# Performance work log

Measured on AMD Instinct MI355X. Metric: run time of the kernel, lower is better.

Reference implementation:

```python
import jax, jax.numpy as jnp
import numpy as np

N_NODES = 100000
N_EDGES = 3200000
D_IN = 256
D_HID = 256
D_OUT = 256


def _sage_conv(x, src, tgt, W_l, b_l, W_r):
    # PyG SAGEConv (aggr='mean', root_weight=True):
    #   out = lin_l(mean_{j in N(i)} x_j) + lin_r(x_i)
    n = x.shape[0]
    msgs = x[src]                                              # [E, d] gather
    agg = jax.ops.segment_sum(msgs, tgt, num_segments=n)       # [N, d] scatter-add
    deg = jax.ops.segment_sum(jnp.ones((src.shape[0],), x.dtype), tgt,
                              num_segments=n)                  # [N]
    agg = agg / jnp.maximum(deg, 1.0)[:, None]                 # mean aggregation
    return agg @ W_l + b_l + x @ W_r


def setup_inputs() -> dict:
    key = jax.random.key(0)
    ks = jax.random.split(key, 8)
    x = jax.random.normal(ks[0], (N_NODES, D_IN), dtype=jnp.float32)
    edge_index = jax.random.randint(ks[1], (2, N_EDGES), 0, N_NODES, dtype=jnp.int64)
    s1 = 1.0 / np.sqrt(D_IN)
    s2 = 1.0 / np.sqrt(D_HID)
    return {
        "x": x,
        "edge_index": edge_index,
        "W_l1": jax.random.uniform(ks[2], (D_IN, D_HID), jnp.float32, -s1, s1),
        "b1": jnp.zeros((D_HID,), jnp.float32),
        "W_r1": jax.random.uniform(ks[3], (D_IN, D_HID), jnp.float32, -s1, s1),
        "W_l2": jax.random.uniform(ks[4], (D_HID, D_OUT), jnp.float32, -s2, s2),
        "b2": jnp.zeros((D_OUT,), jnp.float32),
        "W_r2": jax.random.uniform(ks[5], (D_HID, D_OUT), jnp.float32, -s2, s2),
    }


def reference(x, edge_index, W_l1, b1, W_r1, W_l2, b2, W_r2):
    src, tgt = edge_index[0], edge_index[1]
    h = jax.nn.relu(_sage_conv(x, src, tgt, W_l1, b1, W_r1))   # layer 1 + relu
    # dropout p=0.0 -> identity
    logits = _sage_conv(h, src, tgt, W_l2, b2, W_r2)           # final layer
    return logits
```

## Files before the change

### kernel.cpp

```cpp
#include <hip/hip_runtime.h>
#include <hip/hip_bf16.h>
#include <cstdint>
#include <cstddef>

#define N_NODES 100000
#define N_EDGES 3200000
#define D 256
#define CAP 64
#define OVF_MAX (1 << 20)

typedef __attribute__((ext_vector_type(8))) short short8;
typedef __attribute__((ext_vector_type(4))) float f32x4;

__device__ inline unsigned short f2bf(float f) {
    unsigned int u = __float_as_uint(f);
    u += 0x7FFFu + ((u >> 16) & 1u);
    return (unsigned short)(u >> 16);
}
__device__ inline float bf2f(unsigned short h) {
    return __uint_as_float(((unsigned int)h) << 16);
}

__global__ void fill_bucket(const int* __restrict__ src,
                            const int* __restrict__ tgt,
                            int* __restrict__ cnt,
                            int* __restrict__ bucket,
                            int2* __restrict__ ovf,
                            int* __restrict__ ovf_cnt) {
    int e = blockIdx.x * blockDim.x + threadIdx.x;
    if (e >= N_EDGES) return;
    int t = tgt[e];
    int s = src[e];
    if (t >= 0 && t < N_NODES && s >= 0 && s < N_NODES) {
        int p = atomicAdd(&cnt[t], 1);
        if (p < CAP) {
            bucket[(size_t)t * CAP + p] = s;
        } else {
            int q = atomicAdd(ovf_cnt, 1);
            if (q < OVF_MAX) ovf[q] = make_int2(t, s);
        }
    }
}

__global__ __launch_bounds__(256) void convert_kernel(const float* __restrict__ in,
                                                      unsigned short* __restrict__ out,
                                                      int n8) {
    int i = blockIdx.x * 256 + threadIdx.x;
    if (i >= n8) return;
    const float4 a = ((const float4*)in)[i * 2 + 0];
    const float4 b = ((const float4*)in)[i * 2 + 1];
    short8 v;
    v[0] = (short)f2bf(a.x); v[1] = (short)f2bf(a.y);
    v[2] = (short)f2bf(a.z); v[3] = (short)f2bf(a.w);
    v[4] = (short)f2bf(b.x); v[5] = (short)f2bf(b.y);
    v[6] = (short)f2bf(b.z); v[7] = (short)f2bf(b.w);
    ((short8*)out)[i] = v;
}

__global__ __launch_bounds__(256) void pack_b_kernel(const float* __restrict__ Wl,
                                                     const float* __restrict__ Wr,
                                                     unsigned short* __restrict__ Bp) {
    int t = blockIdx.x * 256 + threadIdx.x;
    if (t >= 16384) return;
    int lane = t & 63, kb = (t >> 6) & 15, ntile = t >> 10;
    int n = ntile * 16 + (lane & 15);
    int kbase = kb * 32 + (lane >> 4) * 8;
    short8 v;
#pragma unroll
    for (int j = 0; j < 8; ++j) {
        int k = kbase + j;
        const float* W = (k < 256) ? Wl : Wr;
        v[j] = (short)f2bf(W[(size_t)(k & 255) * D + n]);
    }
    ((short8*)Bp)[t] = v;
}

__device__ inline void acc8(float& a0, float& a1, float& a2, float& a3,
                            float& a4, float& a5, float& a6, float& a7,
                            const short8& r) {
    a0 += bf2f((unsigned short)r[0]); a1 += bf2f((unsigned short)r[1]);
    a2 += bf2f((unsigned short)r[2]); a3 += bf2f((unsigned short)r[3]);
    a4 += bf2f((unsigned short)r[4]); a5 += bf2f((unsigned short)r[5]);
    a6 += bf2f((unsigned short)r[6]); a7 += bf2f((unsigned short)r[7]);
}

__global__ __launch_bounds__(256) void aggregate_bf16(
    const unsigned short* __restrict__ in, unsigned short* __restrict__ out,
    const int* __restrict__ cnt, const int* __restrict__ bucket,
    const int2* __restrict__ ovf, const int* __restrict__ ovf_cnt) {
    int node = blockIdx.x * 4 + (threadIdx.x >> 6);
    if (node >= N_NODES) return;
    const int lane = threadIdx.x & 63;
    const int half = lane >> 5;
    const int l32  = lane & 31;
    const int deg = cnt[node];
    const int inb = (deg < CAP) ? deg : CAP;
    const int* __restrict__ bk = bucket + (size_t)node * CAP;
    const unsigned short* __restrict__ rowp = in + (size_t)l32 * 8;

    float a0 = 0.f, a1 = 0.f, a2 = 0.f, a3 = 0.f;
    float a4 = 0.f, a5 = 0.f, a6 = 0.f, a7 = 0.f;

    int i0 = (0 + half < inb) ? bk[0 + half] : -1;
    int i1 = (2 + half < inb) ? bk[2 + half] : -1;
    int i2 = (4 + half < inb) ? bk[4 + half] : -1;
    int i3 = (6 + half < inb) ? bk[6 + half] : -1;

    for (int k = 0; k < inb; k += 8) {
        const int kn = k + 8;
        int n0 = (kn + 0 + half < inb) ? bk[kn + 0 + half] : -1;
        int n1 = (kn + 2 + half < inb) ? bk[kn + 2 + half] : -1;
        int n2 = (kn + 4 + half < inb) ? bk[kn + 4 + half] : -1;
        int n3 = (kn + 6 + half < inb) ? bk[kn + 6 + half] : -1;

        short8 r0 = {}, r1 = {}, r2 = {}, r3 = {};
        if (i0 >= 0) r0 = *(const short8*)(rowp + (size_t)i0 * D);
        if (i1 >= 0) r1 = *(const short8*)(rowp + (size_t)i1 * D);
        if (i2 >= 0) r2 = *(const short8*)(rowp + (size_t)i2 * D);
        if (i3 >= 0) r3 = *(const short8*)(rowp + (size_t)i3 * D);

        acc8(a0, a1, a2, a3, a4, a5, a6, a7, r0);
        acc8(a0, a1, a2, a3, a4, a5, a6, a7, r1);
        acc8(a0, a1, a2, a3, a4, a5, a6, a7, r2);
        acc8(a0, a1, a2, a3, a4, a5, a6, a7, r3);

        i0 = n0; i1 = n1; i2 = n2; i3 = n3;
    }

    if (deg > CAP) {
        int m = *ovf_cnt;
        if (m > OVF_MAX) m = OVF_MAX;
        for (int q = half; q < m; q += 2) {
            int2 ts = ovf[q];
            if (ts.x == node) {
                short8 r = *(const short8*)(rowp + (size_t)ts.y * D);
                acc8(a0, a1, a2, a3, a4, a5, a6, a7, r);
            }
        }
    }

    a0 += __shfl_xor(a0, 32); a1 += __shfl_xor(a1, 32);
    a2 += __shfl_xor(a2, 32); a3 += __shfl_xor(a3, 32);
    a4 += __shfl_xor(a4, 32); a5 += __shfl_xor(a5, 32);
    a6 += __shfl_xor(a6, 32); a7 += __shfl_xor(a7, 32);

    if (half == 0) {
        const float inv = 1.0f / fmaxf((float)deg, 1.0f);
        short8 v;
        v[0] = (short)f2bf(a0 * inv); v[1] = (short)f2bf(a1 * inv);
        v[2] = (short)f2bf(a2 * inv); v[3] = (short)f2bf(a3 * inv);
        v[4] = (short)f2bf(a4 * inv); v[5] = (short)f2bf(a5 * inv);
        v[6] = (short)f2bf(a6 * inv); v[7] = (short)f2bf(a7 * inv);
        *(short8*)(out + (size_t)node * D + l32 * 8) = v;
    }
}

__global__ __launch_bounds__(256) void gemm_mfma(
    const unsigned short* __restrict__ A0, const unsigned short* __restrict__ A1,
    const unsigned short* __restrict__ Bp, const float* __restrict__ bias,
    void* __restrict__ outp, int relu, int out_bf16) {
    __shared__ unsigned short As[128][40];
    const int m0 = blockIdx.y * 128;
    const int n0 = blockIdx.x * 128;
    const int t = threadIdx.x;
    const int wave = t >> 6, lane = t & 63;
    const int wy = wave >> 1, wx = wave & 1;
    const int quad = lane >> 4, l16 = lane & 15;

    const int arow = t >> 1;
    const int ahalf = (t & 1) * 16;

    f32x4 acc[4][4] = {};

    for (int kb = 0; kb < 16; ++kb) {
        const int k0 = kb * 32;
        const unsigned short* A = (k0 < 256) ? A0 : A1;
        const int kk = k0 & 255;

        short8 v0 = {}, v1 = {};
        if (m0 + arow < N_NODES) {
            const unsigned short* p = A + (size_t)(m0 + arow) * D + kk + ahalf;
            v0 = *(const short8*)p;
            v1 = *(const short8*)(p + 8);
        }
        *(short8*)&As[arow][ahalf + 0] = v0;
        *(short8*)&As[arow][ahalf + 8] = v1;
        __syncthreads();

        short8 af[4], bf[4];
#pragma unroll
        for (int mi = 0; mi < 4; ++mi)
            af[mi] = *(const short8*)&As[wy * 64 + mi * 16 + l16][quad * 8];
#pragma unroll
        for (int ni = 0; ni < 4; ++ni) {
            int ntile = (n0 >> 4) + wx * 4 + ni;
            bf[ni] = ((const short8*)Bp)[(size_t)(ntile * 16 + kb) * 64 + lane];
        }
#pragma unroll
        for (int mi = 0; mi < 4; ++mi)
#pragma unroll
            for (int ni = 0; ni < 4; ++ni)
                acc[mi][ni] = __builtin_amdgcn_mfma_f32_16x16x32_bf16(
                    af[mi], bf[ni], acc[mi][ni], 0, 0, 0);
        __syncthreads();
    }

    unsigned short* ob = (unsigned short*)outp;
    float* of = (float*)outp;
#pragma unroll
    for (int ni = 0; ni < 4; ++ni) {
        const int col = n0 + wx * 64 + ni * 16 + l16;
        const float bcol = bias[col];
#pragma unroll
        for (int mi = 0; mi < 4; ++mi) {
#pragma unroll
            for (int r = 0; r < 4; ++r) {
                int row = m0 + wy * 64 + mi * 16 + quad * 4 + r;
                if (row < N_NODES) {
                    float v = acc[mi][ni][r] + bcol;
                    if (relu) v = fmaxf(v, 0.f);
                    if (out_bf16) ob[(size_t)row * D + col] = f2bf(v);
                    else          of[(size_t)row * D + col] = v;
                }
            }
        }
    }
}

extern "C" void kernel_launch(void* const* d_in, const int* in_sizes, int n_in,
                              void* d_out, int out_size, void* d_ws, size_t ws_size,
                              hipStream_t stream) {
    const float* x    = (const float*)d_in[0];
    const int*   ei   = (const int*)d_in[1];
    const float* W_l1 = (const float*)d_in[2];
    const float* b1   = (const float*)d_in[3];
    const float* W_r1 = (const float*)d_in[4];
    const float* W_l2 = (const float*)d_in[5];
    const float* b2   = (const float*)d_in[6];
    const float* W_r2 = (const float*)d_in[7];
    float* out = (float*)d_out;

    const int* src = ei;
    const int* tgt = ei + N_EDGES;

    char* w = (char*)d_ws;
    size_t o = 0;
    auto alloc = [&](size_t bytes) {
        size_t p = o;
        o = (o + bytes + 255) & ~(size_t)255;
        return p;
    };
    int*  cnt     = (int*)(w + alloc((size_t)N_NODES * 4));
    int*  ovf_cnt = (int*)(w + alloc(256));
    int*  bucket  = (int*)(w + alloc((size_t)N_NODES * CAP * 4));
    int2* ovf     = (int2*)(w + alloc((size_t)OVF_MAX * 8));
    unsigned short* xb   = (unsigned short*)(w + alloc((size_t)N_NODES * D * 2));
    unsigned short* hb   = (unsigned short*)(w + alloc((size_t)N_NODES * D * 2));
    unsigned short* aggb = (unsigned short*)(w + alloc((size_t)N_NODES * D * 2));
    unsigned short* Bp1  = (unsigned short*)(w + alloc((size_t)512 * D * 2));
    unsigned short* Bp2  = (unsigned short*)(w + alloc((size_t)512 * D * 2));
    (void)ws_size; (void)in_sizes; (void)n_in; (void)out_size;

    hipMemsetAsync(cnt, 0, (size_t)N_NODES * 4, stream);
    hipMemsetAsync(ovf_cnt, 0, 4, stream);

    const int EB = (N_EDGES + 255) / 256;
    fill_bucket<<<EB, 256, 0, stream>>>(src, tgt, cnt, bucket, ovf, ovf_cnt);

    const int n8 = N_NODES * D / 8;
    convert_kernel<<<(n8 + 255) / 256, 256, 0, stream>>>(x, xb, n8);
    pack_b_kernel<<<64, 256, 0, stream>>>(W_l1, W_r1, Bp1);
    pack_b_kernel<<<64, 256, 0, stream>>>(W_l2, W_r2, Bp2);

    const int AGG_B = (N_NODES + 3) / 4;
    dim3 ggrid(2, (N_NODES + 127) / 128);

    aggregate_bf16<<<AGG_B, 256, 0, stream>>>(xb, aggb, cnt, bucket, ovf, ovf_cnt);
    gemm_mfma<<<ggrid, 256, 0, stream>>>(aggb, xb, Bp1, b1, hb, 1, 1);

    aggregate_bf16<<<AGG_B, 256, 0, stream>>>(hb, aggb, cnt, bucket, ovf, ovf_cnt);
    gemm_mfma<<<ggrid, 256, 0, stream>>>(aggb, hb, Bp2, b2, out, 0, 0);
}
```

Measured before the change: 1.077 ms.

## Build CSR via 64-node bins and per-bin local sort instead of per-node buckets

Replaces per-node fixed-capacity buckets (atomic per target node, 64 slots each) with a two-level scheme. Edges are first appended into 64-node bins using padded bin counters, then a single-block scan computes bin offsets, and a per-bin kernel counting-sorts entries in LDS into a compact CSR (offs, sorted_src). This aims to cut heavy per-node atomic contention and the scattered bucket writes, and gives the aggregation compact contiguous neighbor lists. It adds two extra kernels, including a serial single-block scan, and makes every aggregation wave read the overflow counter.

```diff
diff --git a/kernel.cpp b/kernel.cpp
--- a/kernel.cpp
+++ b/kernel.cpp
@@ -6,7 +6,9 @@
 #define N_NODES 100000
 #define N_EDGES 3200000
 #define D 256
-#define CAP 64
+#define NBINS 1563
+#define CAPB 2560
+#define CNT_STRIDE 16
 #define OVF_MAX (1 << 20)
 
 typedef __attribute__((ext_vector_type(8))) short short8;
@@ -21,24 +23,99 @@
     return __uint_as_float(((unsigned int)h) << 16);
 }
 
-__global__ void fill_bucket(const int* __restrict__ src,
-                            const int* __restrict__ tgt,
-                            int* __restrict__ cnt,
-                            int* __restrict__ bucket,
-                            int2* __restrict__ ovf,
-                            int* __restrict__ ovf_cnt) {
+__global__ void binfill_kernel(const int* __restrict__ src,
+                               const int* __restrict__ tgt,
+                               int* __restrict__ bin_cnt,
+                               unsigned int* __restrict__ bin_buf,
+                               int2* __restrict__ ovf,
+                               int* __restrict__ ovf_cnt) {
     int e = blockIdx.x * blockDim.x + threadIdx.x;
     if (e >= N_EDGES) return;
     int t = tgt[e];
     int s = src[e];
     if (t >= 0 && t < N_NODES && s >= 0 && s < N_NODES) {
-        int p = atomicAdd(&cnt[t], 1);
-        if (p < CAP) {
-            bucket[(size_t)t * CAP + p] = s;
+        int b = t >> 6;
+        int p = atomicAdd(&bin_cnt[b * CNT_STRIDE], 1);
+        if (p < CAPB) {
+            bin_buf[(size_t)b * CAPB + p] = ((unsigned int)(t & 63) << 17) | (unsigned int)s;
         } else {
             int q = atomicAdd(ovf_cnt, 1);
             if (q < OVF_MAX) ovf[q] = make_int2(t, s);
         }
+    }
+}
+
+__global__ __launch_bounds__(256) void scan_bins(const int* __restrict__ bin_cnt,
+                                                 int* __restrict__ bin_base,
+                                                 int* __restrict__ offs) {
+    __shared__ int s[256];
+    __shared__ int carry;
+    const int t = threadIdx.x;
+    if (t == 0) carry = 0;
+    __syncthreads();
+    for (int chunk = 0; chunk < (NBINS + 255) / 256; ++chunk) {
+        int b = chunk * 256 + t;
+        int v = 0;
+        if (b < NBINS) {
+            v = bin_cnt[b * CNT_STRIDE];
+            if (v > CAPB) v = CAPB;
+        }
+        s[t] = v;
+        __syncthreads();
+        for (int d = 1; d < 256; d <<= 1) {
+            int x = (t >= d) ? s[t - d] : 0;
+            __syncthreads();
+            s[t] += x;
+            __syncthreads();
+        }
+        if (b < NBINS) bin_base[b] = carry + s[t] - v;
+        __syncthreads();
+        if (t == 0) carry += s[255];
+        __syncthreads();
+    }
+    if (t == 0) {
+        bin_base[NBINS] = carry;
+        offs[N_NODES] = carry;
+    }
+}
+
+__global__ __launch_bounds__(256) void bin_expand(const int* __restrict__ bin_cnt,
+                                                  const int* __restrict__ bin_base,
+                                                  const unsigned int* __restrict__ bin_buf,
+                                                  int* __restrict__ offs,
+                                                  int* __restrict__ sorted_src) {
+    __shared__ unsigned int ent[CAPB];
+    __shared__ int cnt64[64], off64[64], cur64[64];
+    const int b = blockIdx.x;
+    const int tid = threadIdx.x;
+    int n = bin_cnt[b * CNT_STRIDE];
+    if (n > CAPB) n = CAPB;
+    const int base = bin_base[b];
+
+    if (tid < 64) cnt64[tid] = 0;
+    __syncthreads();
+    for (int i = tid; i < n; i += 256) {
+        unsigned int v = bin_buf[(size_t)b * CAPB + i];
+        ent[i] = v;
+        atomicAdd(&cnt64[v >> 17], 1);
+    }
+    __syncthreads();
+    if (tid == 0) {
+        int run = 0;
+#pragma unroll
+        for (int i = 0; i < 64; ++i) { off64[i] = run; run += cnt64[i]; }
+    }
+    __syncthreads();
+    if (tid < 64) {
+        cur64[tid] = off64[tid];
+        int node = b * 64 + tid;
+        if (node < N_NODES) offs[node] = base + off64[tid];
+    }
+    __syncthreads();
+    for (int i = tid; i < n; i += 256) {
+        unsigned int v = ent[i];
+        int p = atomicAdd(&cur64[v >> 17], 1);
+        sorted_src[base + p] = (int)(v & 0x1FFFFu);
     }
 }
 
@@ -86,32 +163,31 @@
 
 __global__ __launch_bounds__(256) void aggregate_bf16(
     const unsigned short* __restrict__ in, unsigned short* __restrict__ out,
-    const int* __restrict__ cnt, const int* __restrict__ bucket,
+    const int* __restrict__ offs, const int* __restrict__ sorted_src,
     const int2* __restrict__ ovf, const int* __restrict__ ovf_cnt) {
     int node = blockIdx.x * 4 + (threadIdx.x >> 6);
     if (node >= N_NODES) return;
     const int lane = threadIdx.x & 63;
     const int half = lane >> 5;
     const int l32  = lane & 31;
-    const int deg = cnt[node];
-    const int inb = (deg < CAP) ? deg : CAP;
-    const int* __restrict__ bk = bucket + (size_t)node * CAP;
+    const int beg = offs[node];
+    const int inb = offs[node + 1] - beg;
     const unsigned short* __restrict__ rowp = in + (size_t)l32 * 8;
 
     float a0 = 0.f, a1 = 0.f, a2 = 0.f, a3 = 0.f;
     float a4 = 0.f, a5 = 0.f, a6 = 0.f, a7 = 0.f;
 
-    int i0 = (0 + half < inb) ? bk[0 + half] : -1;
-    int i1 = (2 + half < inb) ? bk[2 + half] : -1;
-    int i2 = (4 + half < inb) ? bk[4 + half] : -1;
-    int i3 = (6 + half < inb) ? bk[6 + half] : -1;
+    int i0 = (0 + half < inb) ? sorted_src[beg + 0 + half] : -1;
+    int i1 = (2 + half < inb) ? sorted_src[beg + 2 + half] : -1;
+    int i2 = (4 + half < inb) ? sorted_src[beg + 4 + half] : -1;
+    int i3 = (6 + half < inb) ? sorted_src[beg + 6 + half] : -1;
 
     for (int k = 0; k < inb; k += 8) {
         const int kn = k + 8;
-        int n0 = (kn + 0 + half < inb) ? bk[kn + 0 + half] : -1;
-        int n1 = (kn + 2 + half < inb) ? bk[kn + 2 + half] : -1;
-        int n2 = (kn + 4 + half < inb) ? bk[kn + 4 + half] : -1;
-        int n3 = (kn + 6 + half < inb) ? bk[kn + 6 + half] : -1;
+        int n0 = (kn + 0 + half < inb) ? sorted_src[beg + kn + 0 + half] : -1;
+        int n1 = (kn + 2 + half < inb) ? sorted_src[beg + kn + 2 + half] : -1;
+        int n2 = (kn + 4 + half < inb) ? sorted_src[beg + kn + 4 + half] : -1;
+        int n3 = (kn + 6 + half < inb) ? sorted_src[beg + kn + 6 + half] : -1;
 
         short8 r0 = {}, r1 = {}, r2 = {}, r3 = {};
         if (i0 >= 0) r0 = *(const short8*)(rowp + (size_t)i0 * D);
@@ -127,14 +203,16 @@
         i0 = n0; i1 = n1; i2 = n2; i3 = n3;
     }
 
-    if (deg > CAP) {
-        int m = *ovf_cnt;
+    int extra = 0;
+    int m = *ovf_cnt;
+    if (m > 0) {
         if (m > OVF_MAX) m = OVF_MAX;
         for (int q = half; q < m; q += 2) {
             int2 ts = ovf[q];
             if (ts.x == node) {
                 short8 r = *(const short8*)(rowp + (size_t)ts.y * D);
                 acc8(a0, a1, a2, a3, a4, a5, a6, a7, r);
+                ++extra;
             }
         }
     }
@@ -143,9 +221,10 @@
     a2 += __shfl_xor(a2, 32); a3 += __shfl_xor(a3, 32);
     a4 += __shfl_xor(a4, 32); a5 += __shfl_xor(a5, 32);
     a6 += __shfl_xor(a6, 32); a7 += __shfl_xor(a7, 32);
+    extra += __shfl_xor(extra, 32);
 
     if (half == 0) {
-        const float inv = 1.0f / fmaxf((float)deg, 1.0f);
+        const float inv = 1.0f / fmaxf((float)(inb + extra), 1.0f);
         short8 v;
         v[0] = (short)f2bf(a0 * inv); v[1] = (short)f2bf(a1 * inv);
         v[2] = (short)f2bf(a2 * inv); v[3] = (short)f2bf(a3 * inv);
@@ -250,10 +329,13 @@
         o = (o + bytes + 255) & ~(size_t)255;
         return p;
     };
-    int*  cnt     = (int*)(w + alloc((size_t)N_NODES * 4));
-    int*  ovf_cnt = (int*)(w + alloc(256));
-    int*  bucket  = (int*)(w + alloc((size_t)N_NODES * CAP * 4));
-    int2* ovf     = (int2*)(w + alloc((size_t)OVF_MAX * 8));
+    int*  bin_cnt  = (int*)(w + alloc((size_t)NBINS * CNT_STRIDE * 4));
+    int*  bin_base = (int*)(w + alloc((size_t)(NBINS + 1) * 4));
+    int*  ovf_cnt  = (int*)(w + alloc(256));
+    unsigned int* bin_buf = (unsigned int*)(w + alloc((size_t)NBINS * CAPB * 4));
+    int2* ovf      = (int2*)(w + alloc((size_t)OVF_MAX * 8));
+    int*  offs     = (int*)(w + alloc((size_t)(N_NODES + 1) * 4));
+    int*  sorted_src = (int*)(w + alloc((size_t)N_EDGES * 4));
     unsigned short* xb   = (unsigned short*)(w + alloc((size_t)N_NODES * D * 2));
     unsigned short* hb   = (unsigned short*)(w + alloc((size_t)N_NODES * D * 2));
     unsigned short* aggb = (unsigned short*)(w + alloc((size_t)N_NODES * D * 2));
@@ -261,11 +343,13 @@
     unsigned short* Bp2  = (unsigned short*)(w + alloc((size_t)512 * D * 2));
     (void)ws_size; (void)in_sizes; (void)n_in; (void)out_size;
 
-    hipMemsetAsync(cnt, 0, (size_t)N_NODES * 4, stream);
+    hipMemsetAsync(bin_cnt, 0, (size_t)NBINS * CNT_STRIDE * 4, stream);
     hipMemsetAsync(ovf_cnt, 0, 4, stream);
 
     const int EB = (N_EDGES + 255) / 256;
-    fill_bucket<<<EB, 256, 0, stream>>>(src, tgt, cnt, bucket, ovf, ovf_cnt);
+    binfill_kernel<<<EB, 256, 0, stream>>>(src, tgt, bin_cnt, bin_buf, ovf, ovf_cnt);
+    scan_bins<<<1, 256, 0, stream>>>(bin_cnt, bin_base, offs);
+    bin_expand<<<NBINS, 256, 0, stream>>>(bin_cnt, bin_base, bin_buf, offs, sorted_src);
 
     const int n8 = N_NODES * D / 8;
     convert_kernel<<<(n8 + 255) / 256, 256, 0, stream>>>(x, xb, n8);
@@ -275,9 +359,9 @@
     const int AGG_B = (N_NODES + 3) / 4;
     dim3 ggrid(2, (N_NODES + 127) / 128);
 
-    aggregate_bf16<<<AGG_B, 256, 0, stream>>>(xb, aggb, cnt, bucket, ovf, ovf_cnt);
+    aggregate_bf16<<<AGG_B, 256, 0, stream>>>(xb, aggb, offs, sorted_src, ovf, ovf_cnt);
     gemm_mfma<<<ggrid, 256, 0, stream>>>(aggb, xb, Bp1, b1, hb, 1, 1);
 
-    aggregate_bf16<<<AGG_B, 256, 0, stream>>>(hb, aggb, cnt, bucket, ovf, ovf_cnt);
+    aggregate_bf16<<<AGG_B, 256, 0, stream>>>(hb, aggb, offs, sorted_src, ovf, ovf_cnt);
     gemm_mfma<<<ggrid, 256, 0, stream>>>(aggb, hb, Bp2, b2, out, 0, 0);
 }
```

Result: no change. 1.063 ms (-1.3%).
